# Kernel optimization log

Measured on AMD Instinct MI355X. Metric: run time of the kernel, lower is better.

The kernel has to match this reference:

```python
import jax, jax.numpy as jnp
import numpy as np

N, E, G, F0 = 1536, 1536, 64, 12
IN2 = 256 + F0  # 268


def _nnconv(x, src, dst, ea, Wa, ba, Wb, bb, root, bias, n_nodes):
    # edge MLP -> per-edge weight matrix [E, in_ch, out_ch]
    h = jax.nn.leaky_relu(ea @ Wa + ba) @ Wb + bb
    in_ch, out_ch = x.shape[1], root.shape[1]
    W = h.reshape(-1, in_ch, out_ch)
    msg = jnp.einsum('ei,eio->eo', x[src], W)  # gather + batched edge matmul
    s = jax.ops.segment_sum(msg, dst, num_segments=n_nodes)
    c = jax.ops.segment_sum(jnp.ones((dst.shape[0],), msg.dtype), dst, num_segments=n_nodes)
    return s / jnp.maximum(c, 1.0)[:, None] + x @ root + bias


def setup_inputs() -> dict:
    key = jax.random.key(0)
    ks = jax.random.split(key, 32)
    p = lambda k, shape, fan: (jax.random.normal(k, shape, jnp.float32) / np.float32(np.sqrt(fan)))
    inp = {
        'x': jax.random.normal(ks[0], (N, F0), jnp.float32),
        'edge_attr': jax.random.uniform(ks[1], (E, 4), jnp.float32),
        'edge_index': jax.random.randint(ks[2], (2, E), 0, N, jnp.int64),
        'batch': jnp.sort(jax.random.randint(ks[3], (N,), 0, G, jnp.int64)),
        # conv1: edge MLP 4->256->F0*256, root [F0,256]
        'nn1_Wa': p(ks[4], (4, 256), 4), 'nn1_ba': jnp.zeros((256,), jnp.float32),
        'nn1_Wb': p(ks[5], (256, F0 * 256), 256), 'nn1_bb': jnp.zeros((F0 * 256,), jnp.float32),
        'root1': p(ks[6], (F0, 256), F0), 'bias1': jnp.zeros((256,), jnp.float32),
        # conv2: edge MLP 4->512->IN2*256, root [IN2,256]
        'nn2_Wa': p(ks[7], (4, 512), 4), 'nn2_ba': jnp.zeros((512,), jnp.float32),
        'nn2_Wb': p(ks[8], (512, IN2 * 256), 512), 'nn2_bb': jnp.zeros((IN2 * 256,), jnp.float32),
        'root2': p(ks[9], (IN2, 256), IN2), 'bias2': jnp.zeros((256,), jnp.float32),
        # conv3: edge MLP 4->512->IN2*512, root [IN2,512]
        'nn3_Wa': p(ks[10], (4, 512), 4), 'nn3_ba': jnp.zeros((512,), jnp.float32),
        'nn3_Wb': p(ks[11], (512, IN2 * 512), 512), 'nn3_bb': jnp.zeros((IN2 * 512,), jnp.float32),
        'root3': p(ks[12], (IN2, 512), IN2), 'bias3': jnp.zeros((512,), jnp.float32),
        # FC head on pooled [512+F0]
        'fc1_W': p(ks[13], (512 + F0, 768), 512 + F0), 'fc1_b': jnp.zeros((768,), jnp.float32),
        'fc2_W': p(ks[14], (768, 1024), 768), 'fc2_b': jnp.zeros((1024,), jnp.float32),
        'fc3_W': p(ks[15], (1024, 1), 1024), 'fc3_b': jnp.zeros((1,), jnp.float32),
    }
    return inp


def reference(x, edge_attr, edge_index, batch,
              nn1_Wa, nn1_ba, nn1_Wb, nn1_bb, root1, bias1,
              nn2_Wa, nn2_ba, nn2_Wb, nn2_bb, root2, bias2,
              nn3_Wa, nn3_ba, nn3_Wb, nn3_bb, root3, bias3,
              fc1_W, fc1_b, fc2_W, fc2_b, fc3_W, fc3_b):
    src, dst = edge_index[0], edge_index[1]
    n = x.shape[0]
    h1 = jax.nn.leaky_relu(_nnconv(x, src, dst, edge_attr, nn1_Wa, nn1_ba, nn1_Wb, nn1_bb, root1, bias1, n))
    d1 = jnp.concatenate([h1, x], axis=-1)
    h2 = jax.nn.leaky_relu(_nnconv(d1, src, dst, edge_attr, nn2_Wa, nn2_ba, nn2_Wb, nn2_bb, root2, bias2, n))
    d2 = jnp.concatenate([h2, x], axis=-1)
    h3 = jax.nn.leaky_relu(_nnconv(d2, src, dst, edge_attr, nn3_Wa, nn3_ba, nn3_Wb, nn3_bb, root3, bias3, n))
    d3 = jnp.concatenate([h3, x], axis=-1)
    # graph-level scatter-mean pooling
    s = jax.ops.segment_sum(d3, batch, num_segments=G)
    c = jax.ops.segment_sum(jnp.ones((n,), d3.dtype), batch, num_segments=G)
    g = s / jnp.maximum(c, 1.0)[:, None]
    g = jax.nn.leaky_relu(g @ fc1_W + fc1_b)
    g = jax.nn.leaky_relu(g @ fc2_W + fc2_b)
    return g @ fc3_W + fc3_b
```

## Files before the change

### kernel.cpp

```cpp
#include <hip/hip_runtime.h>

#define EN 1536
#define NG 64
#define F0V 12

typedef _Float16 half8_t __attribute__((ext_vector_type(8)));
typedef float f32x16 __attribute__((ext_vector_type(16)));
typedef unsigned int uint4_t __attribute__((ext_vector_type(4)));

__device__ __forceinline__ float lrelu(float v) { return v >= 0.f ? v : 0.01f * v; }

__global__ void k_counts(const int* __restrict__ dst, const int* __restrict__ batch,
                         float* __restrict__ cntE, float* __restrict__ cntg) {
    int t = blockIdx.x * 256 + threadIdx.x;
    if (t < EN) {
        atomicAdd(&cntE[dst[t]], 1.f);
        atomicAdd(&cntg[batch[t]], 1.f);
    }
}

template<int K>
__global__ void k_edge_mlp(const float* __restrict__ ea, const float* __restrict__ Wa,
                           const float* __restrict__ ba, unsigned* __restrict__ zdup) {
    int idx = blockIdx.x * 256 + threadIdx.x;
    int e = idx % EN, k = idx / EN;
    if (k >= K) return;
    float u = ba[k];
#pragma unroll
    for (int a = 0; a < 4; ++a) u += ea[e * 4 + a] * Wa[a * K + k];
    u = lrelu(u);
    _Float16 h = (_Float16)u;
    unsigned short us = __builtin_bit_cast(unsigned short, h);
    zdup[(size_t)k * EN + e] = (unsigned)us * 0x10001u;
}

template<int NIQ, int IC, int IACT>
__global__ void k_gatherw(const float* __restrict__ feat, const int* __restrict__ src,
                          _Float16* __restrict__ xsw) {
    constexpr int NI0 = IC / 16;
    int idx = blockIdx.x * 256 + threadIdx.x;
    int pc = idx & 511, cg = idx >> 9;
    int lane = pc >> 3, j = pc & 7;
    int c2 = cg % (NI0 * 8), tq = cg / (NI0 * 8);
    int iq = tq % NIQ, mt = tq / NIQ;
    int i0 = c2 >> 3, eg = c2 & 7;
    int e = mt * 256 + eg * 32 + (lane & 31);
    int i = iq * IC + i0 * 16 + (lane >> 5) * 8 + j;
    float v = (i < IACT) ? feat[(size_t)src[e] * IACT + i] : 0.f;
    xsw[idx] = (_Float16)v;
}

template<int O, int IACT, int NIQ, int IC>
__global__ void k_swz(const float* __restrict__ Wb, _Float16* __restrict__ Bs) {
    const int k = blockIdx.x, KT = gridDim.x;
    const int nt = blockIdx.y / NIQ, iq = blockIdx.y % NIQ;
    __shared__ float tile[IC * 258];
    const int t = threadIdx.x;
#pragma unroll
    for (int u = 0; u < IC / 8; ++u) {
        int r = u * 8 + (t >> 6), c4 = t & 63;
        int i = iq * IC + r;
        float4 v = {0.f, 0.f, 0.f, 0.f};
        if (i < IACT) v = *(const float4*)(Wb + ((size_t)k * IACT + i) * O + nt * 256 + c4 * 4);
        tile[r * 258 + c4 * 4 + 0] = v.x;
        tile[r * 258 + c4 * 4 + 1] = v.y;
        tile[r * 258 + c4 * 4 + 2] = v.z;
        tile[r * 258 + c4 * 4 + 3] = v.w;
    }
    __syncthreads();
    constexpr int PT = IC * 256 / 512;
    _Float16 ov[PT];
#pragma unroll
    for (int q = 0; q < PT; ++q) {
        int p = t * PT + q;
        int c = p >> 9, pc = p & 511, ln = pc >> 3, j = pc & 7;
        int i0 = c >> 3, g = c & 7;
        int il = i0 * 16 + (ln >> 5) * 8 + j;
        int nl = g * 32 + (ln & 31);
        ov[q] = (_Float16)tile[il * 258 + nl];
    }
    size_t base = ((size_t)blockIdx.y * KT + k) * (size_t)(IC * 256) + (size_t)t * PT;
#pragma unroll
    for (int q8 = 0; q8 < PT / 8; ++q8)
        *(half8_t*)(Bs + base + q8 * 8) = *(const half8_t*)(ov + q8 * 8);
}

template<int IW>
__global__ void k_scatter(const float* __restrict__ feat, const int* __restrict__ src,
                          const int* __restrict__ dst, float* __restrict__ S) {
    int idx = blockIdx.x * 256 + threadIdx.x;
    int e = idx / IW, i = idx % IW;
    atomicAdd(&S[(size_t)dst[e] * IW + i], feat[(size_t)src[e] * IW + i]);
}

template<int KTOT, int O, int NIQ, int IC, int ZMAX>
__global__ __launch_bounds__(512, 2)
void edge_gemm(const _Float16* __restrict__ Bs, const unsigned* __restrict__ zdup,
               const _Float16* __restrict__ xsw, const int* __restrict__ dstIdx,
               float* __restrict__ accG) {
    constexpr int NI0 = IC / 16;
    constexpr int TILEH = IC * 256;
    constexpr int CPW = (TILEH / 512) / 8;

    __shared__ __attribute__((aligned(16))) _Float16 BL[2][TILEH];
    __shared__ unsigned zL[ZMAX * 256];
    __shared__ int dstL[256];

    const int t = threadIdx.x, lane = t & 63, w = t >> 6;
    const int wm = w >> 1, wn = w & 1;
    const int mt = blockIdx.x, nt = blockIdx.y, zb = blockIdx.z, NZ = gridDim.z;
    const int e0 = mt * 256, n0 = nt * 256;
    const int k0 = (KTOT * zb) / NZ, k1 = (KTOT * (zb + 1)) / NZ, kn = k1 - k0;

    if (t < 256) dstL[t] = dstIdx[e0 + t];
    for (int idx = t; idx < kn * 256; idx += 512)
        zL[idx] = zdup[(size_t)(k0 + (idx >> 8)) * EN + e0 + (idx & 255)];

    f32x16 acc[2][4] = {};
    const _Float16* xbase = xsw + (size_t)mt * NIQ * NI0 * 8 * 512;
    half8_t xsr[NI0][2];

    auto dma_issue = [&](const _Float16* srcp, int buf) {
#pragma unroll
        for (int u = 0; u < CPW; ++u) {
            int ch = w * CPW + u;
            __builtin_amdgcn_global_load_lds(
                (__attribute__((address_space(1))) void*)(srcp + ch * 512 + lane * 8),
                (__attribute__((address_space(3))) void*)(&BL[buf][ch * 512]),
                16, 0, 0);
        }
    };

    const _Float16* pB = Bs + ((size_t)(nt * NIQ) * KTOT + k0) * TILEH;
    int kk_n = 0;
    auto adv = [&]() {
        if (++kk_n == kn) { kk_n = 0; pB += (size_t)(KTOT - kn + 1) * TILEH; }
        else pB += (size_t)TILEH;
    };

    const int S = NIQ * kn;
    dma_issue(pB, 0);
    adv();

    int iq = 0, kk = 0;
    for (int s = 0; s < S; ++s) {
        const int buf = s & 1;
        __syncthreads();
        if (s + 1 < S) { dma_issue(pB, buf ^ 1); adv(); }
        if (kk == 0) {
#pragma unroll
            for (int i0 = 0; i0 < NI0; ++i0)
#pragma unroll
                for (int mf = 0; mf < 2; ++mf)
                    xsr[i0][mf] = *(const half8_t*)(xbase +
                        ((size_t)iq * NI0 * 8 + i0 * 8 + wm * 2 + mf) * 512 + lane * 8);
        }
        unsigned zd0 = zL[kk * 256 + wm * 64 + (lane & 31)];
        unsigned zd1 = zL[kk * 256 + wm * 64 + 32 + (lane & 31)];
        uint4_t u0 = {zd0, zd0, zd0, zd0}, u1 = {zd1, zd1, zd1, zd1};
        half8_t z0 = __builtin_bit_cast(half8_t, u0);
        half8_t z1 = __builtin_bit_cast(half8_t, u1);
#pragma unroll
        for (int i0 = 0; i0 < NI0; ++i0) {
            half8_t a0 = xsr[i0][0] * z0;
            half8_t a1 = xsr[i0][1] * z1;
#pragma unroll
            for (int nf = 0; nf < 4; ++nf) {
                half8_t b = *(const half8_t*)(&BL[buf][(i0 * 8 + wn * 4 + nf) * 512 + lane * 8]);
                acc[0][nf] = __builtin_amdgcn_mfma_f32_32x32x16_f16(a0, b, acc[0][nf], 0, 0, 0);
                acc[1][nf] = __builtin_amdgcn_mfma_f32_32x32x16_f16(a1, b, acc[1][nf], 0, 0, 0);
            }
        }
        if (++kk == kn) { kk = 0; ++iq; }
    }

#pragma unroll
    for (int mf = 0; mf < 2; ++mf)
#pragma unroll
        for (int nf = 0; nf < 4; ++nf)
#pragma unroll
            for (int r = 0; r < 16; ++r) {
                int row = (r & 3) + 8 * (r >> 2) + 4 * (lane >> 5);
                int m = wm * 64 + mf * 32 + row;
                int o = wn * 128 + nf * 32 + (lane & 31);
                atomicAdd(&accG[(size_t)dstL[m] * O + n0 + o], acc[mf][nf][r]);
            }
}

template<int O, int IW>
__global__ void k_combine(const float* __restrict__ acc, const float* __restrict__ S,
                          const float* __restrict__ dprev, const float* __restrict__ bb,
                          const float* __restrict__ root, const float* __restrict__ bias,
                          const float* __restrict__ cntE, const float* __restrict__ x,
                          float* __restrict__ dL) {
    int idx = blockIdx.x * 256 + threadIdx.x;
    int n = idx / O, o = idx % O;
    float sbb = 0.f, rt = 0.f;
    for (int i = 0; i < IW; ++i) {
        sbb = fmaf(S[(size_t)n * IW + i], bb[(size_t)i * O + o], sbb);
        rt  = fmaf(dprev[(size_t)n * IW + i], root[(size_t)i * O + o], rt);
    }
    float c = fmaxf(cntE[n], 1.f);
    float v = (acc[(size_t)n * O + o] + sbb) / c + rt + bias[o];
    v = lrelu(v);
    dL[(size_t)n * (O + F0V) + o] = v;
    if (o < F0V) dL[(size_t)n * (O + F0V) + O + o] = x[n * F0V + o];
}

__global__ void k_pool(const float* __restrict__ d3, const int* __restrict__ batch,
                       float* __restrict__ pooled) {
    int idx = blockIdx.x * 256 + threadIdx.x;
    int n = idx / 524, j = idx % 524;
    atomicAdd(&pooled[(size_t)batch[n] * 524 + j], d3[idx]);
}

template<int IN, int OUT, bool LEAKY, bool DIV>
__global__ void k_fc(const float* __restrict__ in, const float* __restrict__ W,
                     const float* __restrict__ b, const float* __restrict__ cnt,
                     float* __restrict__ out) {
    int idx = blockIdx.x * blockDim.x + threadIdx.x;
    if (idx >= NG * OUT) return;
    int g = idx & 63, o = idx >> 6;
    float v = 0.f;
    for (int i = 0; i < IN; ++i) v = fmaf(in[(size_t)g * IN + i], W[(size_t)i * OUT + o], v);
    if (DIV) v /= fmaxf(cnt[g], 1.f);
    v += b[o];
    if (LEAKY) v = lrelu(v);
    out[(size_t)g * OUT + o] = v;
}

extern "C" void kernel_launch(void* const* d_in, const int* in_sizes, int n_in,
                              void* d_out, int out_size, void* d_ws, size_t ws_size,
                              hipStream_t stream) {
    const float* x     = (const float*)d_in[0];
    const float* ea    = (const float*)d_in[1];
    const int*   ei    = (const int*)d_in[2];
    const int*   batch = (const int*)d_in[3];
    const float* W1a = (const float*)d_in[4];  const float* b1a = (const float*)d_in[5];
    const float* W1b = (const float*)d_in[6];  const float* b1b = (const float*)d_in[7];
    const float* root1 = (const float*)d_in[8]; const float* bias1 = (const float*)d_in[9];
    const float* W2a = (const float*)d_in[10]; const float* b2a = (const float*)d_in[11];
    const float* W2b = (const float*)d_in[12]; const float* b2b = (const float*)d_in[13];
    const float* root2 = (const float*)d_in[14]; const float* bias2 = (const float*)d_in[15];
    const float* W3a = (const float*)d_in[16]; const float* b3a = (const float*)d_in[17];
    const float* W3b = (const float*)d_in[18]; const float* b3b = (const float*)d_in[19];
    const float* root3 = (const float*)d_in[20]; const float* bias3 = (const float*)d_in[21];
    const float* fc1W = (const float*)d_in[22]; const float* fc1b = (const float*)d_in[23];
    const float* fc2W = (const float*)d_in[24]; const float* fc2b = (const float*)d_in[25];
    const float* fc3W = (const float*)d_in[26]; const float* fc3b = (const float*)d_in[27];
    const int* src = ei;
    const int* dst = ei + EN;
    float* out = (float*)d_out;

    char* wp = (char*)d_ws;
    auto alloc = [&](size_t bytes) { char* p = wp; wp += (bytes + 511) & ~(size_t)511; return p; };
    unsigned* zdup1 = (unsigned*)alloc((size_t)256 * EN * 4);
    unsigned* zdup2 = (unsigned*)alloc((size_t)512 * EN * 4);
    unsigned* zdup3 = (unsigned*)alloc((size_t)512 * EN * 4);
    _Float16* xsw1 = (_Float16*)alloc((size_t)EN * 16 * 2);
    _Float16* xsw2 = (_Float16*)alloc((size_t)EN * 320 * 2);
    _Float16* xsw3 = (_Float16*)alloc((size_t)EN * 320 * 2);
    _Float16* Bs = (_Float16*)alloc((size_t)10 * 512 * 16384 * 2);
    float* d1 = (float*)alloc((size_t)EN * 268 * 4);
    float* d2 = (float*)alloc((size_t)EN * 268 * 4);
    float* d3 = (float*)alloc((size_t)EN * 524 * 4);
    float* acc = (float*)alloc((size_t)EN * 512 * 4);
    float* S = (float*)alloc((size_t)EN * 268 * 4);
    float* cntE = (float*)alloc((size_t)EN * 4);
    float* cntg = (float*)alloc((size_t)NG * 4);
    float* pooled = (float*)alloc((size_t)NG * 524 * 4);
    float* fc1o = (float*)alloc((size_t)NG * 768 * 4);
    float* fc2o = (float*)alloc((size_t)NG * 1024 * 4);

    hipMemsetAsync(cntE, 0, (size_t)EN * 4, stream);
    hipMemsetAsync(cntg, 0, (size_t)NG * 4, stream);
    k_counts<<<6, 256, 0, stream>>>(dst, batch, cntE, cntg);

    k_edge_mlp<256><<<256 * EN / 256, 256, 0, stream>>>(ea, W1a, b1a, zdup1);
    k_edge_mlp<512><<<512 * EN / 256, 256, 0, stream>>>(ea, W2a, b2a, zdup2);
    k_edge_mlp<512><<<512 * EN / 256, 256, 0, stream>>>(ea, W3a, b3a, zdup3);

    k_gatherw<1, 16, 12><<<EN * 16 / 256, 256, 0, stream>>>(x, src, xsw1);
    k_swz<256, 12, 1, 16><<<dim3(256, 1), 512, 0, stream>>>(W1b, Bs);
    hipMemsetAsync(S, 0, (size_t)EN * 12 * 4, stream);
    k_scatter<12><<<EN * 12 / 256, 256, 0, stream>>>(x, src, dst, S);
    hipMemsetAsync(acc, 0, (size_t)EN * 256 * 4, stream);
    edge_gemm<256, 256, 1, 16, 8><<<dim3(6, 1, 42), 512, 0, stream>>>(Bs, zdup1, xsw1, dst, acc);
    k_combine<256, 12><<<EN * 256 / 256, 256, 0, stream>>>(acc, S, x, b1b, root1, bias1, cntE, x, d1);

    k_gatherw<5, 64, 268><<<EN * 320 / 256, 256, 0, stream>>>(d1, src, xsw2);
    k_swz<256, 268, 5, 64><<<dim3(512, 5), 512, 0, stream>>>(W2b, Bs);
    hipMemsetAsync(S, 0, (size_t)EN * 268 * 4, stream);
    k_scatter<268><<<EN * 268 / 256, 256, 0, stream>>>(d1, src, dst, S);
    hipMemsetAsync(acc, 0, (size_t)EN * 256 * 4, stream);
    edge_gemm<512, 256, 5, 64, 14><<<dim3(6, 1, 42), 512, 0, stream>>>(Bs, zdup2, xsw2, dst, acc);
    k_combine<256, 268><<<EN * 256 / 256, 256, 0, stream>>>(acc, S, d1, b2b, root2, bias2, cntE, x, d2);

    k_gatherw<5, 64, 268><<<EN * 320 / 256, 256, 0, stream>>>(d2, src, xsw3);
    k_swz<512, 268, 5, 64><<<dim3(512, 10), 512, 0, stream>>>(W3b, Bs);
    hipMemsetAsync(S, 0, (size_t)EN * 268 * 4, stream);
    k_scatter<268><<<EN * 268 / 256, 256, 0, stream>>>(d2, src, dst, S);
    hipMemsetAsync(acc, 0, (size_t)EN * 512 * 4, stream);
    edge_gemm<512, 512, 5, 64, 26><<<dim3(6, 2, 21), 512, 0, stream>>>(Bs, zdup3, xsw3, dst, acc);
    k_combine<512, 268><<<EN * 512 / 256, 256, 0, stream>>>(acc, S, d2, b3b, root3, bias3, cntE, x, d3);

    hipMemsetAsync(pooled, 0, (size_t)NG * 524 * 4, stream);
    k_pool<<<EN * 524 / 256, 256, 0, stream>>>(d3, batch, pooled);
    k_fc<524, 768, true, true><<<NG * 768 / 256, 256, 0, stream>>>(pooled, fc1W, fc1b, cntg, fc1o);
    k_fc<768, 1024, true, false><<<NG * 1024 / 256, 256, 0, stream>>>(fc1o, fc2W, fc2b, nullptr, fc2o);
    k_fc<1024, 1, false, false><<<1, 64, 0, stream>>>(fc2o, fc3W, fc3b, nullptr, out);
}
```

Before: 1.433 ms.

## Narrow edge GEMM tiles, fuse scatter into gather, merge memsets, parallelize fc3

The edge GEMM now uses 128-wide N tiles with 256-thread blocks, and the input channel chunk shrinks from 64 to 32. This cuts zero padding of the 268-wide input from 320 to 288 columns and gives more blocks. The per-edge feature scatter-add is folded into the gather kernel, and the acc/S and count memsets are merged into single calls. The final FC layer becomes a per-graph block reduction instead of a single 64-thread block. The trade-off is more weight-tile reloads and more output atomics per block, and the merged memsets rely on the workspace buffers being contiguous.

```diff
diff --git a/kernel.cpp b/kernel.cpp
--- a/kernel.cpp
+++ b/kernel.cpp
@@ -36,7 +36,8 @@
 
 template<int NIQ, int IC, int IACT>
 __global__ void k_gatherw(const float* __restrict__ feat, const int* __restrict__ src,
-                          _Float16* __restrict__ xsw) {
+                          const int* __restrict__ dst, _Float16* __restrict__ xsw,
+                          float* __restrict__ S) {
     constexpr int NI0 = IC / 16;
     int idx = blockIdx.x * 256 + threadIdx.x;
     int pc = idx & 511, cg = idx >> 9;
@@ -46,7 +47,11 @@
     int i0 = c2 >> 3, eg = c2 & 7;
     int e = mt * 256 + eg * 32 + (lane & 31);
     int i = iq * IC + i0 * 16 + (lane >> 5) * 8 + j;
-    float v = (i < IACT) ? feat[(size_t)src[e] * IACT + i] : 0.f;
+    float v = 0.f;
+    if (i < IACT) {
+        v = feat[(size_t)src[e] * IACT + i];
+        atomicAdd(&S[(size_t)dst[e] * IACT + i], v);
+    }
     xsw[idx] = (_Float16)v;
 }
 
@@ -54,66 +59,57 @@
 __global__ void k_swz(const float* __restrict__ Wb, _Float16* __restrict__ Bs) {
     const int k = blockIdx.x, KT = gridDim.x;
     const int nt = blockIdx.y / NIQ, iq = blockIdx.y % NIQ;
-    __shared__ float tile[IC * 258];
+    __shared__ float tile[IC * 132];
     const int t = threadIdx.x;
 #pragma unroll
     for (int u = 0; u < IC / 8; ++u) {
-        int r = u * 8 + (t >> 6), c4 = t & 63;
+        int r = u * 8 + (t >> 5), c4 = t & 31;
         int i = iq * IC + r;
         float4 v = {0.f, 0.f, 0.f, 0.f};
-        if (i < IACT) v = *(const float4*)(Wb + ((size_t)k * IACT + i) * O + nt * 256 + c4 * 4);
-        tile[r * 258 + c4 * 4 + 0] = v.x;
-        tile[r * 258 + c4 * 4 + 1] = v.y;
-        tile[r * 258 + c4 * 4 + 2] = v.z;
-        tile[r * 258 + c4 * 4 + 3] = v.w;
+        if (i < IACT) v = *(const float4*)(Wb + ((size_t)k * IACT + i) * O + nt * 128 + c4 * 4);
+        tile[r * 132 + c4 * 4 + 0] = v.x;
+        tile[r * 132 + c4 * 4 + 1] = v.y;
+        tile[r * 132 + c4 * 4 + 2] = v.z;
+        tile[r * 132 + c4 * 4 + 3] = v.w;
     }
     __syncthreads();
-    constexpr int PT = IC * 256 / 512;
+    constexpr int PT = IC * 128 / 256;
     _Float16 ov[PT];
 #pragma unroll
     for (int q = 0; q < PT; ++q) {
         int p = t * PT + q;
         int c = p >> 9, pc = p & 511, ln = pc >> 3, j = pc & 7;
-        int i0 = c >> 3, g = c & 7;
+        int i0 = c >> 2, g = c & 3;
         int il = i0 * 16 + (ln >> 5) * 8 + j;
         int nl = g * 32 + (ln & 31);
-        ov[q] = (_Float16)tile[il * 258 + nl];
-    }
-    size_t base = ((size_t)blockIdx.y * KT + k) * (size_t)(IC * 256) + (size_t)t * PT;
+        ov[q] = (_Float16)tile[il * 132 + nl];
+    }
+    size_t base = ((size_t)blockIdx.y * KT + k) * (size_t)(IC * 128) + (size_t)t * PT;
 #pragma unroll
     for (int q8 = 0; q8 < PT / 8; ++q8)
         *(half8_t*)(Bs + base + q8 * 8) = *(const half8_t*)(ov + q8 * 8);
 }
 
-template<int IW>
-__global__ void k_scatter(const float* __restrict__ feat, const int* __restrict__ src,
-                          const int* __restrict__ dst, float* __restrict__ S) {
-    int idx = blockIdx.x * 256 + threadIdx.x;
-    int e = idx / IW, i = idx % IW;
-    atomicAdd(&S[(size_t)dst[e] * IW + i], feat[(size_t)src[e] * IW + i]);
-}
-
 template<int KTOT, int O, int NIQ, int IC, int ZMAX>
-__global__ __launch_bounds__(512, 2)
+__global__ __launch_bounds__(256, 2)
 void edge_gemm(const _Float16* __restrict__ Bs, const unsigned* __restrict__ zdup,
                const _Float16* __restrict__ xsw, const int* __restrict__ dstIdx,
                float* __restrict__ accG) {
     constexpr int NI0 = IC / 16;
-    constexpr int TILEH = IC * 256;
-    constexpr int CPW = (TILEH / 512) / 8;
+    constexpr int TILEH = IC * 128;
+    constexpr int CPW = NI0;
 
     __shared__ __attribute__((aligned(16))) _Float16 BL[2][TILEH];
     __shared__ unsigned zL[ZMAX * 256];
     __shared__ int dstL[256];
 
-    const int t = threadIdx.x, lane = t & 63, w = t >> 6;
-    const int wm = w >> 1, wn = w & 1;
+    const int t = threadIdx.x, lane = t & 63, wm = t >> 6;
     const int mt = blockIdx.x, nt = blockIdx.y, zb = blockIdx.z, NZ = gridDim.z;
-    const int e0 = mt * 256, n0 = nt * 256;
+    const int e0 = mt * 256, n0 = nt * 128;
     const int k0 = (KTOT * zb) / NZ, k1 = (KTOT * (zb + 1)) / NZ, kn = k1 - k0;
 
-    if (t < 256) dstL[t] = dstIdx[e0 + t];
-    for (int idx = t; idx < kn * 256; idx += 512)
+    dstL[t] = dstIdx[e0 + t];
+    for (int idx = t; idx < kn * 256; idx += 256)
         zL[idx] = zdup[(size_t)(k0 + (idx >> 8)) * EN + e0 + (idx & 255)];
 
     f32x16 acc[2][4] = {};
@@ -123,7 +119,7 @@
     auto dma_issue = [&](const _Float16* srcp, int buf) {
 #pragma unroll
         for (int u = 0; u < CPW; ++u) {
-            int ch = w * CPW + u;
+            int ch = wm * CPW + u;
             __builtin_amdgcn_global_load_lds(
                 (__attribute__((address_space(1))) void*)(srcp + ch * 512 + lane * 8),
                 (__attribute__((address_space(3))) void*)(&BL[buf][ch * 512]),
@@ -153,7 +149,7 @@
 #pragma unroll
                 for (int mf = 0; mf < 2; ++mf)
                     xsr[i0][mf] = *(const half8_t*)(xbase +
-                        ((size_t)iq * NI0 * 8 + i0 * 8 + wm * 2 + mf) * 512 + lane * 8);
+                        ((size_t)(iq * NI0 + i0) * 8 + wm * 2 + mf) * 512 + lane * 8);
         }
         unsigned zd0 = zL[kk * 256 + wm * 64 + (lane & 31)];
         unsigned zd1 = zL[kk * 256 + wm * 64 + 32 + (lane & 31)];
@@ -166,7 +162,7 @@
             half8_t a1 = xsr[i0][1] * z1;
 #pragma unroll
             for (int nf = 0; nf < 4; ++nf) {
-                half8_t b = *(const half8_t*)(&BL[buf][(i0 * 8 + wn * 4 + nf) * 512 + lane * 8]);
+                half8_t b = *(const half8_t*)(&BL[buf][(i0 * 4 + nf) * 512 + lane * 8]);
                 acc[0][nf] = __builtin_amdgcn_mfma_f32_32x32x16_f16(a0, b, acc[0][nf], 0, 0, 0);
                 acc[1][nf] = __builtin_amdgcn_mfma_f32_32x32x16_f16(a1, b, acc[1][nf], 0, 0, 0);
             }
@@ -182,7 +178,7 @@
             for (int r = 0; r < 16; ++r) {
                 int row = (r & 3) + 8 * (r >> 2) + 4 * (lane >> 5);
                 int m = wm * 64 + mf * 32 + row;
-                int o = wn * 128 + nf * 32 + (lane & 31);
+                int o = nf * 32 + (lane & 31);
                 atomicAdd(&accG[(size_t)dstL[m] * O + n0 + o], acc[mf][nf][r]);
             }
 }
@@ -227,6 +223,21 @@
     v += b[o];
     if (LEAKY) v = lrelu(v);
     out[(size_t)g * OUT + o] = v;
+}
+
+__global__ void k_fc3r(const float* __restrict__ in, const float* __restrict__ W,
+                       const float* __restrict__ b, float* __restrict__ out) {
+    __shared__ float red[256];
+    int g = blockIdx.x, t = threadIdx.x;
+    float v = 0.f;
+    for (int i = t; i < 1024; i += 256) v = fmaf(in[(size_t)g * 1024 + i], W[i], v);
+    red[t] = v;
+    __syncthreads();
+    for (int s = 128; s > 0; s >>= 1) {
+        if (t < s) red[t] += red[t + s];
+        __syncthreads();
+    }
+    if (t == 0) out[g] = red[0] + b[0];
 }
 
 extern "C" void kernel_launch(void* const* d_in, const int* in_sizes, int n_in,
@@ -258,9 +269,9 @@
     unsigned* zdup2 = (unsigned*)alloc((size_t)512 * EN * 4);
     unsigned* zdup3 = (unsigned*)alloc((size_t)512 * EN * 4);
     _Float16* xsw1 = (_Float16*)alloc((size_t)EN * 16 * 2);
-    _Float16* xsw2 = (_Float16*)alloc((size_t)EN * 320 * 2);
-    _Float16* xsw3 = (_Float16*)alloc((size_t)EN * 320 * 2);
-    _Float16* Bs = (_Float16*)alloc((size_t)10 * 512 * 16384 * 2);
+    _Float16* xsw2 = (_Float16*)alloc((size_t)EN * 288 * 2);
+    _Float16* xsw3 = (_Float16*)alloc((size_t)EN * 288 * 2);
+    _Float16* Bs = (_Float16*)alloc((size_t)4 * 9 * 512 * 4096 * 2);
     float* d1 = (float*)alloc((size_t)EN * 268 * 4);
     float* d2 = (float*)alloc((size_t)EN * 268 * 4);
     float* d3 = (float*)alloc((size_t)EN * 524 * 4);
@@ -271,42 +282,36 @@
     float* pooled = (float*)alloc((size_t)NG * 524 * 4);
     float* fc1o = (float*)alloc((size_t)NG * 768 * 4);
     float* fc2o = (float*)alloc((size_t)NG * 1024 * 4);
-
-    hipMemsetAsync(cntE, 0, (size_t)EN * 4, stream);
-    hipMemsetAsync(cntg, 0, (size_t)NG * 4, stream);
+    const size_t accS_bytes = ((size_t)EN * 512 * 4 + 511 & ~(size_t)511) + (size_t)EN * 268 * 4;
+
+    hipMemsetAsync(cntE, 0, ((size_t)EN * 4 + 511 & ~(size_t)511) + NG * 4, stream);
     k_counts<<<6, 256, 0, stream>>>(dst, batch, cntE, cntg);
 
     k_edge_mlp<256><<<256 * EN / 256, 256, 0, stream>>>(ea, W1a, b1a, zdup1);
     k_edge_mlp<512><<<512 * EN / 256, 256, 0, stream>>>(ea, W2a, b2a, zdup2);
     k_edge_mlp<512><<<512 * EN / 256, 256, 0, stream>>>(ea, W3a, b3a, zdup3);
 
-    k_gatherw<1, 16, 12><<<EN * 16 / 256, 256, 0, stream>>>(x, src, xsw1);
-    k_swz<256, 12, 1, 16><<<dim3(256, 1), 512, 0, stream>>>(W1b, Bs);
-    hipMemsetAsync(S, 0, (size_t)EN * 12 * 4, stream);
-    k_scatter<12><<<EN * 12 / 256, 256, 0, stream>>>(x, src, dst, S);
-    hipMemsetAsync(acc, 0, (size_t)EN * 256 * 4, stream);
-    edge_gemm<256, 256, 1, 16, 8><<<dim3(6, 1, 42), 512, 0, stream>>>(Bs, zdup1, xsw1, dst, acc);
+    hipMemsetAsync(acc, 0, accS_bytes, stream);
+    k_gatherw<1, 16, 12><<<EN * 16 / 256, 256, 0, stream>>>(x, src, dst, xsw1, S);
+    k_swz<256, 12, 1, 16><<<dim3(256, 2), 256, 0, stream>>>(W1b, Bs);
+    edge_gemm<256, 256, 1, 16, 7><<<dim3(6, 2, 42), 256, 0, stream>>>(Bs, zdup1, xsw1, dst, acc);
     k_combine<256, 12><<<EN * 256 / 256, 256, 0, stream>>>(acc, S, x, b1b, root1, bias1, cntE, x, d1);
 
-    k_gatherw<5, 64, 268><<<EN * 320 / 256, 256, 0, stream>>>(d1, src, xsw2);
-    k_swz<256, 268, 5, 64><<<dim3(512, 5), 512, 0, stream>>>(W2b, Bs);
-    hipMemsetAsync(S, 0, (size_t)EN * 268 * 4, stream);
-    k_scatter<268><<<EN * 268 / 256, 256, 0, stream>>>(d1, src, dst, S);
-    hipMemsetAsync(acc, 0, (size_t)EN * 256 * 4, stream);
-    edge_gemm<512, 256, 5, 64, 14><<<dim3(6, 1, 42), 512, 0, stream>>>(Bs, zdup2, xsw2, dst, acc);
+    hipMemsetAsync(acc, 0, accS_bytes, stream);
+    k_gatherw<9, 32, 268><<<EN * 288 / 256, 256, 0, stream>>>(d1, src, dst, xsw2, S);
+    k_swz<256, 268, 9, 32><<<dim3(512, 18), 256, 0, stream>>>(W2b, Bs);
+    edge_gemm<512, 256, 9, 32, 13><<<dim3(6, 2, 42), 256, 0, stream>>>(Bs, zdup2, xsw2, dst, acc);
     k_combine<256, 268><<<EN * 256 / 256, 256, 0, stream>>>(acc, S, d1, b2b, root2, bias2, cntE, x, d2);
 
-    k_gatherw<5, 64, 268><<<EN * 320 / 256, 256, 0, stream>>>(d2, src, xsw3);
-    k_swz<512, 268, 5, 64><<<dim3(512, 10), 512, 0, stream>>>(W3b, Bs);
-    hipMemsetAsync(S, 0, (size_t)EN * 268 * 4, stream);
-    k_scatter<268><<<EN * 268 / 256, 256, 0, stream>>>(d2, src, dst, S);
-    hipMemsetAsync(acc, 0, (size_t)EN * 512 * 4, stream);
-    edge_gemm<512, 512, 5, 64, 26><<<dim3(6, 2, 21), 512, 0, stream>>>(Bs, zdup3, xsw3, dst, acc);
+    hipMemsetAsync(acc, 0, accS_bytes, stream);
+    k_gatherw<9, 32, 268><<<EN * 288 / 256, 256, 0, stream>>>(d2, src, dst, xsw3, S);
+    k_swz<512, 268, 9, 32><<<dim3(512, 36), 256, 0, stream>>>(W3b, Bs);
+    edge_gemm<512, 512, 9, 32, 25><<<dim3(6, 4, 21), 256, 0, stream>>>(Bs, zdup3, xsw3, dst, acc);
     k_combine<512, 268><<<EN * 512 / 256, 256, 0, stream>>>(acc, S, d2, b3b, root3, bias3, cntE, x, d3);
 
     hipMemsetAsync(pooled, 0, (size_t)NG * 524 * 4, stream);
     k_pool<<<EN * 524 / 256, 256, 0, stream>>>(d3, batch, pooled);
     k_fc<524, 768, true, true><<<NG * 768 / 256, 256, 0, stream>>>(pooled, fc1W, fc1b, cntg, fc1o);
     k_fc<768, 1024, true, false><<<NG * 1024 / 256, 256, 0, stream>>>(fc1o, fc2W, fc2b, nullptr, fc2o);
-    k_fc<1024, 1, false, false><<<1, 64, 0, stream>>>(fc2o, fc3W, fc3b, nullptr, out);
-}
+    k_fc3r<<<NG, 256, 0, stream>>>(fc2o, fc3W, fc3b, out);
+}
```

Measured after the change: 1.337 ms. -6.7%, faster.
